# Kernel tuning notes

Measured on AMD Instinct MI355X. Metric: run time of the kernel, lower is better.

Reference implementation:

```python
import jax, jax.numpy as jnp
import numpy as np

B = 131072
SD, AD, HID = 24, 8, 32
NH = SD + AD            # n_heads = 32
UNITS = HID * NH        # 1024


def _xavier(k, shape):
    fan_in, fan_out = shape[-2], shape[-1]
    lim = float(np.sqrt(6.0 / (fan_in + fan_out)))
    return jax.random.uniform(k, shape, jnp.float32, -lim, lim)


def setup_inputs() -> dict:
    key = jax.random.key(0)
    ks = jax.random.split(key, 8)
    return dict(
        state=jax.random.normal(ks[0], (B, SD), jnp.float32),
        action=jax.random.normal(ks[1], (B, AD), jnp.float32),
        # ripple layer 1: per-head Linear(NH -> HID), gate logits init 0 (init_prob=0.5)
        W1=_xavier(ks[2], (NH, NH, HID)), b1=jnp.zeros((NH, HID), jnp.float32), g1=jnp.zeros((NH,), jnp.float32),
        # ripple layer 2: per-head Linear(UNITS -> HID)
        W2=_xavier(ks[3], (NH, UNITS, HID)), b2=jnp.zeros((NH, HID), jnp.float32), g2=jnp.zeros((NH,), jnp.float32),
        # q_network
        Wq1=_xavier(ks[4], (UNITS, 256)), bq1=jnp.zeros((256,), jnp.float32),
        ln1_g=jnp.ones((256,), jnp.float32), ln1_b=jnp.zeros((256,), jnp.float32),
        Wq2=_xavier(ks[5], (256, 128)), bq2=jnp.zeros((128,), jnp.float32),
        ln2_g=jnp.ones((128,), jnp.float32), ln2_b=jnp.zeros((128,), jnp.float32),
        Wq3=_xavier(ks[6], (128, 1)), bq3=jnp.zeros((1,), jnp.float32),
    )


def _ripple(x, W, b, g):
    # x: [B, D]; W: [H, D, K]; per-head linear + tanh, scaled by per-head sigmoid gate
    h = jnp.tanh(jnp.einsum('bd,hdk->bhk', x, W) + b[None])  # [B, H, K]
    h = h * jax.nn.sigmoid(g)[None, :, None]
    return h.reshape(x.shape[0], -1)  # [B, H*K]


def _ln(x, g, b, eps=1e-5):
    mu = jnp.mean(x, -1, keepdims=True)
    var = jnp.mean((x - mu) ** 2, -1, keepdims=True)
    return (x - mu) * jax.lax.rsqrt(var + eps) * g + b


def reference(state, action, W1, b1, g1, W2, b2, g2,
              Wq1, bq1, ln1_g, ln1_b, Wq2, bq2, ln2_g, ln2_b, Wq3, bq3):
    sa = jnp.concatenate([state, action], axis=1)          # [B, SD+AD]
    x = _ripple(sa, W1, b1, g1)                            # [B, UNITS]
    x = _ripple(x, W2, b2, g2)                             # [B, UNITS]
    h = jax.nn.relu(_ln(x @ Wq1 + bq1, ln1_g, ln1_b))      # [B, 256] (dropout = eval identity)
    h = jax.nn.relu(_ln(h @ Wq2 + bq2, ln2_g, ln2_b))      # [B, 128]
    return h @ Wq3 + bq3                                   # [B, 1]
```

## Files before the change

kernel.cpp:

```cpp
#include <hip/hip_runtime.h>
#include <hip/hip_bf16.h>

typedef _Float16 f16x8 __attribute__((ext_vector_type(8)));
typedef _Float16 f16x4 __attribute__((ext_vector_type(4)));
typedef float f32x4 __attribute__((ext_vector_type(4)));

__device__ __forceinline__ float tanh_fast(float x) {
  float e = __expf(2.0f * x);
  return 1.0f - 2.0f * __builtin_amdgcn_rcpf(e + 1.0f);
}
__device__ __forceinline__ float sigmoid_fast(float x) {
  return __builtin_amdgcn_rcpf(1.0f + __expf(-x));
}

__global__ __launch_bounds__(256) void prep_weights(
    const float* __restrict__ W1, const float* __restrict__ W2,
    const float* __restrict__ Wq1, const float* __restrict__ Wq2,
    _Float16* __restrict__ V1p, _Float16* __restrict__ V2p,
    _Float16* __restrict__ T1p, _Float16* __restrict__ T2p) {
  __shared__ float S[32 * 33];
  int b = blockIdx.x, t = threadIdx.x;
  if (b < 2624) {
    const float* in; _Float16* out; int N, nc0, tile;
    if (b < 2048) {
      int h = b >> 6, rem = b & 63, ntl = rem >> 5, kt = rem & 31;
      in = W2 + (size_t)h * 32768 + (size_t)kt * 32 * 32;
      N = 32; nc0 = ntl * 16;
      out = V2p; tile = kt * 64 + (h * 2 + ntl);
    } else if (b < 2560) {
      int i = b - 2048, nt = i >> 5, kt = i & 31;
      in = Wq1 + (size_t)kt * 32 * 256; N = 256; nc0 = nt * 16;
      out = T1p; tile = kt * 16 + nt;
    } else {
      int i = b - 2560, nt = i >> 3, kt = i & 7;
      in = Wq2 + (size_t)kt * 32 * 128; N = 128; nc0 = nt * 16;
      out = T2p; tile = nt * 8 + kt;
    }
    if (t < 128) {
      int r = t >> 2, c4 = (t & 3) * 4;
      const float4 v = *(const float4*)(in + (size_t)r * N + nc0 + c4);
      S[r * 17 + c4 + 0] = v.x; S[r * 17 + c4 + 1] = v.y;
      S[r * 17 + c4 + 2] = v.z; S[r * 17 + c4 + 3] = v.w;
    }
    __syncthreads();
    if (t < 128) {
      int w2 = t >> 6, l = t & 63, q = l >> 4, l15 = l & 15;
      f16x4 o;
#pragma unroll
      for (int jj = 0; jj < 4; ++jj)
        o[jj] = (_Float16)S[(q * 8 + w2 * 4 + jj) * 17 + l15];
      *(f16x4*)(out + (size_t)tile * 512 + l * 8 + w2 * 4) = o;
    }
  } else {
    int h = b - 2624;
    const float* in = W1 + h * 1024;
    int cc = t & 31, rr8 = t >> 5;
#pragma unroll
    for (int p = 0; p < 4; ++p) {
      int r = rr8 + p * 8;
      S[cc * 33 + r] = in[r * 32 + cc];
    }
    __syncthreads();
    if (t < 128) {
      int ntl = t >> 6, l = t & 63, q = l >> 4, l15 = l & 15;
      f16x8 o;
#pragma unroll
      for (int j = 0; j < 8; ++j)
        o[j] = (_Float16)S[(ntl * 16 + l15) * 33 + q * 8 + j];
      *(f16x8*)(V1p + (size_t)(h * 2 + ntl) * 512 + l * 8) = o;
    }
  }
}

__global__ __launch_bounds__(256) void k1_ripple1(
    const float* __restrict__ state, const float* __restrict__ action,
    const _Float16* __restrict__ v1p, const float* __restrict__ b1,
    const float* __restrict__ g1, _Float16* __restrict__ x1p, int gro,
    int NRT, int xcdMatch) {
  __shared__ __align__(16) _Float16 SM[128 * 68];
  int g = blockIdx.x, bn, bm;
  if (xcdMatch) { int x = g & 7, r = g >> 3; bn = r & 7; bm = x + 8 * (r >> 3); }
  else { bn = g & 7; bm = g >> 3; }
  int t = threadIdx.x, w = t >> 6, l = t & 63, q = l >> 4, l15 = l & 15;
  int n0 = bn * 128, m0 = bm * 128;

  {
    int r = t >> 1, half = t & 1;
    size_t grow = (size_t)(gro + m0 + r);
    float v[16];
    if (half == 0) {
      const float4* sp = (const float4*)(state + grow * 24);
      ((float4*)v)[0] = sp[0]; ((float4*)v)[1] = sp[1];
      ((float4*)v)[2] = sp[2]; ((float4*)v)[3] = sp[3];
    } else {
      const float4* sp = (const float4*)(state + grow * 24 + 16);
      ((float4*)v)[0] = sp[0]; ((float4*)v)[1] = sp[1];
      const float4* ap = (const float4*)(action + grow * 8);
      ((float4*)v)[2] = ap[0]; ((float4*)v)[3] = ap[1];
    }
    f16x8 h0, h1;
#pragma unroll
    for (int j = 0; j < 8; ++j) { h0[j] = (_Float16)v[j]; h1[j] = (_Float16)v[8 + j]; }
    *(f16x8*)&SM[r * 40 + half * 16] = h0;
    *(f16x8*)&SM[r * 40 + half * 16 + 8] = h1;
  }
  __syncthreads();

  int wr = w >> 1, wc = w & 1;
  f16x8 af[4], bf[4];
#pragma unroll
  for (int mi = 0; mi < 4; ++mi)
    af[mi] = *(const f16x8*)&SM[(wr * 64 + mi * 16 + l15) * 40 + q * 8];
#pragma unroll
  for (int ni = 0; ni < 4; ++ni)
    bf[ni] = *(const f16x8*)(v1p + (size_t)(bn * 8 + wc * 4 + ni) * 512 + l * 8);

  f32x4 acc[4][4] = {};
#pragma unroll
  for (int mi = 0; mi < 4; ++mi)
#pragma unroll
    for (int ni = 0; ni < 4; ++ni)
      acc[mi][ni] = __builtin_amdgcn_mfma_f32_16x16x32_f16(af[mi], bf[ni], acc[mi][ni], 0, 0, 0);

  for (int p = 0; p < 2; ++p) {
    __syncthreads();
    if (wc == p) {
#pragma unroll
      for (int ni = 0; ni < 4; ++ni) {
        int col = n0 + p * 64 + ni * 16 + l15;
        float sg = sigmoid_fast(g1[col >> 5]);
        float bias = b1[col];
#pragma unroll
        for (int mi = 0; mi < 4; ++mi)
#pragma unroll
          for (int r = 0; r < 4; ++r) {
            int rl = wr * 64 + mi * 16 + q * 4 + r;
            SM[rl * 68 + ni * 16 + l15] = (_Float16)(tanh_fast(acc[mi][ni][r] + bias) * sg);
          }
      }
    }
    __syncthreads();
#pragma unroll
    for (int i = 0; i < 4; ++i) {
      int c = t + i * 256;
      int kcL = c >> 9, rt = (c >> 6) & 7, ll = c & 63;
      int qq = ll >> 4, ll15 = ll & 15;
      int base = (rt * 16 + ll15) * 68 + kcL * 32 + qq * 8;
      union { f16x8 v; f16x4 h[2]; } u;
      u.h[0] = *(const f16x4*)&SM[base];
      u.h[1] = *(const f16x4*)&SM[base + 4];
      int kc = bn * 4 + p * 2 + kcL;
      *(f16x8*)(x1p + ((size_t)kc * NRT + (m0 >> 4) + rt) * 512 + ll * 8) = u.v;
    }
  }
}

__global__ __launch_bounds__(256, 2) void k2_ripple2(
    const _Float16* __restrict__ x1p, const _Float16* __restrict__ v2p,
    const float* __restrict__ b2, const float* __restrict__ g2,
    _Float16* __restrict__ x2p, int nbm, int NRT) {
  __shared__ __align__(16) _Float16 EP[4 * 64 * 36];
  int g = blockIdx.x;
  int bn, bm;
  if ((nbm & 7) == 0) {
    int x = g & 7, j = g >> 3, jj = j >> 2, nJ = nbm >> 3;
    bn = j & 3; bm = x + 8 * (nJ - 1 - jj);
  } else { bn = g & 3; bm = g >> 2; }
  int t = threadIdx.x, w = t >> 6, l = t & 63, q = l >> 4, l15 = l & 15;
  int wr = w >> 1, wc = w & 1;
  int rt0 = bm * 8 + wr * 4;
  int nt0 = bn * 16 + wc * 8;
  f32x4 acc[4][8] = {};

  const size_t aStep = (size_t)NRT * 512;
  const _Float16* aP = x1p + (size_t)rt0 * 512 + (size_t)l * 8;
  const _Float16* bP = v2p + (size_t)nt0 * 512 + (size_t)l * 8;

  f16x8 a0[4], a1[4], b0[8], b1[8];
#pragma unroll
  for (int mi = 0; mi < 4; ++mi) a0[mi] = *(const f16x8*)(aP + mi * 512);
#pragma unroll
  for (int ni = 0; ni < 8; ++ni) b0[ni] = *(const f16x8*)(bP + ni * 512);
#pragma unroll
  for (int mi = 0; mi < 4; ++mi) a1[mi] = *(const f16x8*)(aP + aStep + mi * 512);
#pragma unroll
  for (int ni = 0; ni < 8; ++ni) b1[ni] = *(const f16x8*)(bP + 32768 + ni * 512);
  aP += 2 * aStep; bP += 65536;

  for (int kt = 0; kt < 32; kt += 2) {
#pragma unroll
    for (int mi = 0; mi < 4; ++mi)
#pragma unroll
      for (int ni = 0; ni < 8; ++ni)
        acc[mi][ni] = __builtin_amdgcn_mfma_f32_16x16x32_f16(a0[mi], b0[ni], acc[mi][ni], 0, 0, 0);
    if (kt < 30) {
#pragma unroll
      for (int mi = 0; mi < 4; ++mi) a0[mi] = *(const f16x8*)(aP + mi * 512);
#pragma unroll
      for (int ni = 0; ni < 8; ++ni) b0[ni] = *(const f16x8*)(bP + ni * 512);
    }
#pragma unroll
    for (int mi = 0; mi < 4; ++mi)
#pragma unroll
      for (int ni = 0; ni < 8; ++ni)
        acc[mi][ni] = __builtin_amdgcn_mfma_f32_16x16x32_f16(a1[mi], b1[ni], acc[mi][ni], 0, 0, 0);
    if (kt < 30) {
#pragma unroll
      for (int mi = 0; mi < 4; ++mi) a1[mi] = *(const f16x8*)(aP + aStep + mi * 512);
#pragma unroll
      for (int ni = 0; ni < 8; ++ni) b1[ni] = *(const f16x8*)(bP + 32768 + ni * 512);
      aP += 2 * aStep; bP += 65536;
    }
  }

  _Float16* EPw = EP + w * (64 * 36);
  for (int kcg = 0; kcg < 4; ++kcg) {
#pragma unroll
    for (int np = 0; np < 2; ++np) {
      int ni = kcg * 2 + np;
      int col = (nt0 + ni) * 16 + l15;
      float sg = sigmoid_fast(g2[col >> 5]);
      float bias = b2[col];
#pragma unroll
      for (int mi = 0; mi < 4; ++mi)
#pragma unroll
        for (int r = 0; r < 4; ++r) {
          int row = mi * 16 + q * 4 + r;
          EPw[row * 36 + np * 16 + l15] = (_Float16)(tanh_fast(acc[mi][ni][r] + bias) * sg);
        }
    }
#pragma unroll
    for (int rt = 0; rt < 4; ++rt) {
      int base = (rt * 16 + l15) * 36 + q * 8;
      union { f16x8 v; f16x4 h[2]; } u;
      u.h[0] = *(const f16x4*)&EPw[base];
      u.h[1] = *(const f16x4*)&EPw[base + 4];
      int kc = (nt0 >> 1) + kcg;
      *(f16x8*)(x2p + ((size_t)kc * NRT + rt0 + rt) * 512 + l * 8) = u.v;
    }
  }
}

__global__ __launch_bounds__(512, 3) void k3_head(
    const _Float16* __restrict__ x2p, const _Float16* __restrict__ t1p,
    const _Float16* __restrict__ t2p,
    const float* __restrict__ bq1, const float* __restrict__ ln1g, const float* __restrict__ ln1b,
    const float* __restrict__ bq2, const float* __restrict__ ln2g, const float* __restrict__ ln2b,
    const float* __restrict__ wq3, const float* __restrict__ bq3,
    float* __restrict__ out, int NRT, int SROWS) {
  __shared__ __align__(16) _Float16 y1h[128 * 264];
  __shared__ float redA[128 * 4], redB[128 * 4];
  __shared__ float meanv[128], rstdv[128];
  int bm = blockIdx.x;
  int t = threadIdx.x, w = t >> 6, l = t & 63, q = l >> 4, l15 = l & 15;
  int wr = w >> 2, wc = w & 3;

  int gt = bm * 8;
  int slice = 0;
  if (gt >= NRT) { slice = 1; gt -= NRT; }
  int rt0 = gt + wr * 4;

  f32x4 acc[4][4] = {};
  const size_t aStep = (size_t)NRT * 512;
  const _Float16* aP = x2p + (size_t)slice * SROWS * 1024 + (size_t)rt0 * 512 + (size_t)l * 8;
  const _Float16* bP = t1p + (size_t)(wc * 4) * 512 + (size_t)l * 8;

  f16x8 a0[4], a1[4], b0[4], b1[4];
#pragma unroll
  for (int mi = 0; mi < 4; ++mi) a0[mi] = *(const f16x8*)(aP + mi * 512);
#pragma unroll
  for (int ni = 0; ni < 4; ++ni) b0[ni] = *(const f16x8*)(bP + ni * 512);
#pragma unroll
  for (int mi = 0; mi < 4; ++mi) a1[mi] = *(const f16x8*)(aP + aStep + mi * 512);
#pragma unroll
  for (int ni = 0; ni < 4; ++ni) b1[ni] = *(const f16x8*)(bP + 8192 + ni * 512);
  aP += 2 * aStep; bP += 16384;

  for (int kt = 0; kt < 32; kt += 2) {
#pragma unroll
    for (int mi = 0; mi < 4; ++mi)
#pragma unroll
      for (int ni = 0; ni < 4; ++ni)
        acc[mi][ni] = __builtin_amdgcn_mfma_f32_16x16x32_f16(a0[mi], b0[ni], acc[mi][ni], 0, 0, 0);
    if (kt < 30) {
#pragma unroll
      for (int mi = 0; mi < 4; ++mi) a0[mi] = *(const f16x8*)(aP + mi * 512);
#pragma unroll
      for (int ni = 0; ni < 4; ++ni) b0[ni] = *(const f16x8*)(bP + ni * 512);
    }
#pragma unroll
    for (int mi = 0; mi < 4; ++mi)
#pragma unroll
      for (int ni = 0; ni < 4; ++ni)
        acc[mi][ni] = __builtin_amdgcn_mfma_f32_16x16x32_f16(a1[mi], b1[ni], acc[mi][ni], 0, 0, 0);
    if (kt < 30) {
#pragma unroll
      for (int mi = 0; mi < 4; ++mi) a1[mi] = *(const f16x8*)(aP + aStep + mi * 512);
#pragma unroll
      for (int ni = 0; ni < 4; ++ni) b1[ni] = *(const f16x8*)(bP + 8192 + ni * 512);
      aP += 2 * aStep; bP += 16384;
    }
  }

#pragma unroll
  for (int ni = 0; ni < 4; ++ni) {
    int col = wc * 64 + ni * 16 + l15;
    float b = bq1[col];
#pragma unroll
    for (int mi = 0; mi < 4; ++mi)
#pragma unroll
      for (int r = 0; r < 4; ++r) acc[mi][ni][r] += b;
  }
#pragma unroll
  for (int mi = 0; mi < 4; ++mi)
#pragma unroll
    for (int r = 0; r < 4; ++r) {
      int row = wr * 64 + mi * 16 + q * 4 + r;
      float s = 0.f, sq = 0.f;
#pragma unroll
      for (int ni = 0; ni < 4; ++ni) { float v = acc[mi][ni][r]; s += v; sq += v * v; }
#pragma unroll
      for (int off = 1; off < 16; off <<= 1) { s += __shfl_xor(s, off); sq += __shfl_xor(sq, off); }
      if (l15 == 0) { redA[row * 4 + wc] = s; redB[row * 4 + wc] = sq; }
    }
  __syncthreads();
  if (t < 128) {
    float s  = redA[t * 4] + redA[t * 4 + 1] + redA[t * 4 + 2] + redA[t * 4 + 3];
    float sq = redB[t * 4] + redB[t * 4 + 1] + redB[t * 4 + 2] + redB[t * 4 + 3];
    float mean = s * (1.0f / 256.0f);
    float var = sq * (1.0f / 256.0f) - mean * mean;
    meanv[t] = mean; rstdv[t] = rsqrtf(var + 1e-5f);
  }
  __syncthreads();
#pragma unroll
  for (int mi = 0; mi < 4; ++mi)
#pragma unroll
    for (int ni = 0; ni < 4; ++ni)
#pragma unroll
      for (int r = 0; r < 4; ++r) {
        int row = wr * 64 + mi * 16 + q * 4 + r;
        int col = wc * 64 + ni * 16 + l15;
        float y = (acc[mi][ni][r] - meanv[row]) * rstdv[row] * ln1g[col] + ln1b[col];
        y = fmaxf(y, 0.f);
        y1h[row * 264 + col] = (_Float16)y;
      }
  __syncthreads();

  f32x4 a2[4][2] = {};
  for (int kt = 0; kt < 8; ++kt) {
    f16x8 af2[4];
#pragma unroll
    for (int mi = 0; mi < 4; ++mi)
      af2[mi] = *(const f16x8*)&y1h[(wr * 64 + mi * 16 + l15) * 264 + kt * 32 + q * 8];
#pragma unroll
    for (int ni = 0; ni < 2; ++ni) {
      f16x8 bf = *(const f16x8*)(t2p + (size_t)(wc * 2 + ni) * 4096 + kt * 512 + l * 8);
#pragma unroll
      for (int mi = 0; mi < 4; ++mi)
        a2[mi][ni] = __builtin_amdgcn_mfma_f32_16x16x32_f16(af2[mi], bf, a2[mi][ni], 0, 0, 0);
    }
  }
#pragma unroll
  for (int ni = 0; ni < 2; ++ni) {
    int col = wc * 32 + ni * 16 + l15;
    float b = bq2[col];
#pragma unroll
    for (int mi = 0; mi < 4; ++mi)
#pragma unroll
      for (int r = 0; r < 4; ++r) a2[mi][ni][r] += b;
  }
  __syncthreads();
#pragma unroll
  for (int mi = 0; mi < 4; ++mi)
#pragma unroll
    for (int r = 0; r < 4; ++r) {
      int row = wr * 64 + mi * 16 + q * 4 + r;
      float s = 0.f, sq = 0.f;
#pragma unroll
      for (int ni = 0; ni < 2; ++ni) { float v = a2[mi][ni][r]; s += v; sq += v * v; }
#pragma unroll
      for (int off = 1; off < 16; off <<= 1) { s += __shfl_xor(s, off); sq += __shfl_xor(sq, off); }
      if (l15 == 0) { redA[row * 4 + wc] = s; redB[row * 4 + wc] = sq; }
    }
  __syncthreads();
  if (t < 128) {
    float s  = redA[t * 4] + redA[t * 4 + 1] + redA[t * 4 + 2] + redA[t * 4 + 3];
    float sq = redB[t * 4] + redB[t * 4 + 1] + redB[t * 4 + 2] + redB[t * 4 + 3];
    float mean = s * (1.0f / 128.0f);
    float var = sq * (1.0f / 128.0f) - mean * mean;
    meanv[t] = mean; rstdv[t] = rsqrtf(var + 1e-5f);
  }
  __syncthreads();
#pragma unroll
  for (int mi = 0; mi < 4; ++mi)
#pragma unroll
    for (int r = 0; r < 4; ++r) {
      int row = wr * 64 + mi * 16 + q * 4 + r;
      float pr = 0.f;
#pragma unroll
      for (int ni = 0; ni < 2; ++ni) {
        int col = wc * 32 + ni * 16 + l15;
        float y = (a2[mi][ni][r] - meanv[row]) * rstdv[row] * ln2g[col] + ln2b[col];
        y = fmaxf(y, 0.f);
        pr += y * wq3[col];
      }
#pragma unroll
      for (int off = 1; off < 16; off <<= 1) pr += __shfl_xor(pr, off);
      if (l15 == 0) redA[row * 4 + wc] = pr;
    }
  __syncthreads();
  if (t < 128)
    out[bm * 128 + t] = redA[t * 4] + redA[t * 4 + 1] + redA[t * 4 + 2] + redA[t * 4 + 3] + bq3[0];
}

extern "C" void kernel_launch(void* const* d_in, const int* in_sizes, int n_in,
                              void* d_out, int out_size, void* d_ws, size_t ws_size,
                              hipStream_t stream) {
  const float* state  = (const float*)d_in[0];
  const float* action = (const float*)d_in[1];
  const float* W1  = (const float*)d_in[2];
  const float* b1  = (const float*)d_in[3];
  const float* g1  = (const float*)d_in[4];
  const float* W2  = (const float*)d_in[5];
  const float* b2  = (const float*)d_in[6];
  const float* g2  = (const float*)d_in[7];
  const float* Wq1 = (const float*)d_in[8];
  const float* bq1 = (const float*)d_in[9];
  const float* ln1g = (const float*)d_in[10];
  const float* ln1b = (const float*)d_in[11];
  const float* Wq2 = (const float*)d_in[12];
  const float* bq2 = (const float*)d_in[13];
  const float* ln2g = (const float*)d_in[14];
  const float* ln2b = (const float*)d_in[15];
  const float* Wq3 = (const float*)d_in[16];
  const float* bq3 = (const float*)d_in[17];
  int B = in_sizes[0] / 24;

  char* ws = (char*)d_ws;
  _Float16* V1p = (_Float16*)(ws);
  _Float16* V2p = (_Float16*)(ws + 65536);
  _Float16* T1p = (_Float16*)(ws + 65536 + 2097152);
  _Float16* T2p = (_Float16*)(ws + 65536 + 2097152 + 524288);
  size_t woff = (65536 + 2097152 + 524288 + 65536 + 4095) & ~(size_t)4095;

  size_t avail = ws_size > woff ? ws_size - woff : 0;
  int S, G;
  if (avail >= (size_t)32768 * 2048 * 3) {
    S = 32768; G = 2;
  } else {
    long rows = (long)(avail / 4096);
    if (rows > 32768) rows = 32768;
    rows &= ~127L;
    if (rows < 128) rows = 128;
    S = (int)rows; G = 1;
  }
  _Float16* x1 = (_Float16*)(ws + woff);
  _Float16* x2 = x1 + (size_t)S * 1024;
  int NRT = S / 16;

  prep_weights<<<2656, 256, 0, stream>>>(W1, W2, Wq1, Wq2, V1p, V2p, T1p, T2p);

  int nsl = (B + S - 1) / S;
  for (int i = 0; i < nsl; ++i) {
    int r0 = i * S;
    int Sc = S < (B - r0) ? S : (B - r0);
    int nbm = Sc / 128;
    int xm = (nbm & 7) == 0 ? 1 : 0;
    k1_ripple1<<<dim3(8 * nbm), 256, 0, stream>>>(state, action, V1p, b1, g1, x1, r0,
                                                  NRT, xm);
    k2_ripple2<<<dim3(4 * nbm), 256, 0, stream>>>(x1, V2p, b2, g2,
                                                  x2 + (size_t)(i % G) * S * 1024, nbm, NRT);
    if (i % G == G - 1 || i == nsl - 1) {
      int gstart = (i - i % G) * S;
      int nrows = r0 + Sc - gstart;
      k3_head<<<dim3(nrows / 128), 512, 0, stream>>>(x2, T1p, T2p, bq1, ln1g, ln1b,
                                                     bq2, ln2g, ln2b, Wq3, bq3,
                                                     (float*)d_out + gstart, NRT, S);
    }
  }
}
```

Measured before the change: 636.7 us.

## Fuse ripple layer 1 into ripple layer 2 kernel, keeping x1 in LDS

Merges the two ripple kernels into one 512-thread kernel. Each block recomputes the layer-1 activations for its 128 rows, one 128-column chunk at a time, into double-buffered LDS and feeds them straight into the layer-2 MFMA accumulation. This removes the global write and read of the fp16 x1 intermediate and one kernel launch, and halves the workspace needed per slice. In exchange, layer 1 is recomputed by both column-half blocks, LDS use is much larger and there is a barrier per chunk, which may lower occupancy and latency hiding.

Measured after the change: 608.5 us. 1.05x faster.

```diff
diff --git a/kernel.cpp b/kernel.cpp
--- a/kernel.cpp
+++ b/kernel.cpp
@@ -72,148 +72,123 @@
   }
 }
 
-__global__ __launch_bounds__(256) void k1_ripple1(
+__global__ __launch_bounds__(512, 2) void k12_fused(
     const float* __restrict__ state, const float* __restrict__ action,
     const _Float16* __restrict__ v1p, const float* __restrict__ b1,
-    const float* __restrict__ g1, _Float16* __restrict__ x1p, int gro,
-    int NRT, int xcdMatch) {
-  __shared__ __align__(16) _Float16 SM[128 * 68];
-  int g = blockIdx.x, bn, bm;
-  if (xcdMatch) { int x = g & 7, r = g >> 3; bn = r & 7; bm = x + 8 * (r >> 3); }
-  else { bn = g & 7; bm = g >> 3; }
+    const float* __restrict__ g1,
+    const _Float16* __restrict__ v2p, const float* __restrict__ b2,
+    const float* __restrict__ g2,
+    _Float16* __restrict__ x2p, int gro, int NRT) {
+  __shared__ __align__(16) _Float16 SA[128 * 40];
+  __shared__ __align__(16) _Float16 XF[2 * 16384];
+  __shared__ __align__(16) _Float16 EP[8 * 64 * 36];
+  int g = blockIdx.x;
+  int bn = g & 1, bm = g >> 1;
   int t = threadIdx.x, w = t >> 6, l = t & 63, q = l >> 4, l15 = l & 15;
-  int n0 = bn * 128, m0 = bm * 128;
+  int wrow = w & 1;
+  int cg = w >> 1;
+  int m0 = bm * 128;
 
   {
-    int r = t >> 1, half = t & 1;
+    int r = t >> 2, q4 = t & 3;
     size_t grow = (size_t)(gro + m0 + r);
-    float v[16];
-    if (half == 0) {
-      const float4* sp = (const float4*)(state + grow * 24);
+    float v[8];
+    if (q4 < 3) {
+      const float4* sp = (const float4*)(state + grow * 24 + q4 * 8);
       ((float4*)v)[0] = sp[0]; ((float4*)v)[1] = sp[1];
-      ((float4*)v)[2] = sp[2]; ((float4*)v)[3] = sp[3];
     } else {
-      const float4* sp = (const float4*)(state + grow * 24 + 16);
-      ((float4*)v)[0] = sp[0]; ((float4*)v)[1] = sp[1];
       const float4* ap = (const float4*)(action + grow * 8);
-      ((float4*)v)[2] = ap[0]; ((float4*)v)[3] = ap[1];
-    }
-    f16x8 h0, h1;
-#pragma unroll
-    for (int j = 0; j < 8; ++j) { h0[j] = (_Float16)v[j]; h1[j] = (_Float16)v[8 + j]; }
-    *(f16x8*)&SM[r * 40 + half * 16] = h0;
-    *(f16x8*)&SM[r * 40 + half * 16 + 8] = h1;
-  }
-  __syncthreads();
-
-  int wr = w >> 1, wc = w & 1;
-  f16x8 af[4], bf[4];
-#pragma unroll
-  for (int mi = 0; mi < 4; ++mi)
-    af[mi] = *(const f16x8*)&SM[(wr * 64 + mi * 16 + l15) * 40 + q * 8];
-#pragma unroll
-  for (int ni = 0; ni < 4; ++ni)
-    bf[ni] = *(const f16x8*)(v1p + (size_t)(bn * 8 + wc * 4 + ni) * 512 + l * 8);
-
-  f32x4 acc[4][4] = {};
-#pragma unroll
-  for (int mi = 0; mi < 4; ++mi)
-#pragma unroll
-    for (int ni = 0; ni < 4; ++ni)
-      acc[mi][ni] = __builtin_amdgcn_mfma_f32_16x16x32_f16(af[mi], bf[ni], acc[mi][ni], 0, 0, 0);
-
-  for (int p = 0; p < 2; ++p) {
+      ((float4*)v)[0] = ap[0]; ((float4*)v)[1] = ap[1];
+    }
+    f16x8 h0;
+#pragma unroll
+    for (int j = 0; j < 8; ++j) h0[j] = (_Float16)v[j];
+    *(f16x8*)&SA[r * 40 + q4 * 8] = h0;
+  }
+  __syncthreads();
+
+  f32x4 acc[4][8] = {};
+  _Float16* EPw = EP + w * (64 * 36);
+
+  f16x8 rb[2];
+#pragma unroll
+  for (int ni = 0; ni < 2; ++ni)
+    rb[ni] = *(const f16x8*)(v1p + (size_t)(cg * 2 + ni) * 512 + l * 8);
+
+  const int nt0 = bn * 32 + cg * 8;
+  const _Float16* bBase = v2p + (size_t)nt0 * 512 + (size_t)l * 8;
+
+  for (int kc = 0; kc < 8; ++kc) {
+    f16x8 asa[4];
+#pragma unroll
+    for (int mi = 0; mi < 4; ++mi)
+      asa[mi] = *(const f16x8*)&SA[(wrow * 64 + mi * 16 + l15) * 40 + q * 8];
+    f32x4 a1[4][2] = {};
+#pragma unroll
+    for (int mi = 0; mi < 4; ++mi)
+#pragma unroll
+      for (int ni = 0; ni < 2; ++ni)
+        a1[mi][ni] = __builtin_amdgcn_mfma_f32_16x16x32_f16(asa[mi], rb[ni], a1[mi][ni], 0, 0, 0);
+#pragma unroll
+    for (int ni = 0; ni < 2; ++ni) {
+      int col = kc * 128 + cg * 32 + ni * 16 + l15;
+      float sg = sigmoid_fast(g1[col >> 5]);
+      float bias = b1[col];
+#pragma unroll
+      for (int mi = 0; mi < 4; ++mi)
+#pragma unroll
+        for (int r = 0; r < 4; ++r)
+          EPw[(mi * 16 + q * 4 + r) * 36 + ni * 16 + l15] =
+              (_Float16)(tanh_fast(a1[mi][ni][r] + bias) * sg);
+    }
+    _Float16* buf = XF + (kc & 1) * 16384;
+#pragma unroll
+    for (int rtl = 0; rtl < 4; ++rtl) {
+      int base = (rtl * 16 + l15) * 36 + q * 8;
+      union { f16x8 v; f16x4 h[2]; } u;
+      u.h[0] = *(const f16x4*)&EPw[base];
+      u.h[1] = *(const f16x4*)&EPw[base + 4];
+      *(f16x8*)(buf + ((cg * 8 + wrow * 4 + rtl) * 64 + l) * 8) = u.v;
+    }
     __syncthreads();
-    if (wc == p) {
-#pragma unroll
-      for (int ni = 0; ni < 4; ++ni) {
-        int col = n0 + p * 64 + ni * 16 + l15;
-        float sg = sigmoid_fast(g1[col >> 5]);
-        float bias = b1[col];
-#pragma unroll
-        for (int mi = 0; mi < 4; ++mi)
-#pragma unroll
-          for (int r = 0; r < 4; ++r) {
-            int rl = wr * 64 + mi * 16 + q * 4 + r;
-            SM[rl * 68 + ni * 16 + l15] = (_Float16)(tanh_fast(acc[mi][ni][r] + bias) * sg);
-          }
+
+    if (kc < 7) {
+#pragma unroll
+      for (int ni = 0; ni < 2; ++ni)
+        rb[ni] = *(const f16x8*)(v1p + (size_t)((kc + 1) * 8 + cg * 2 + ni) * 512 + l * 8);
+    }
+    int ktg = kc * 4;
+    f16x8 bb0[8], bb1[8];
+#pragma unroll
+    for (int ni = 0; ni < 8; ++ni)
+      bb0[ni] = *(const f16x8*)(bBase + (size_t)(ktg * 64 + ni) * 512);
+#pragma unroll
+    for (int ni = 0; ni < 8; ++ni)
+      bb1[ni] = *(const f16x8*)(bBase + (size_t)((ktg + 1) * 64 + ni) * 512);
+#pragma unroll
+    for (int ktL = 0; ktL < 4; ++ktL) {
+      f16x8 af[4];
+#pragma unroll
+      for (int mi = 0; mi < 4; ++mi)
+        af[mi] = *(const f16x8*)(buf + ((ktL * 8 + wrow * 4 + mi) * 64 + l) * 8);
+      f16x8* bb = (ktL & 1) ? bb1 : bb0;
+#pragma unroll
+      for (int mi = 0; mi < 4; ++mi)
+#pragma unroll
+        for (int ni = 0; ni < 8; ++ni)
+          acc[mi][ni] = __builtin_amdgcn_mfma_f32_16x16x32_f16(af[mi], bb[ni], acc[mi][ni], 0, 0, 0);
+      if (ktL == 0) {
+#pragma unroll
+        for (int ni = 0; ni < 8; ++ni)
+          bb0[ni] = *(const f16x8*)(bBase + (size_t)((ktg + 2) * 64 + ni) * 512);
+      } else if (ktL == 1) {
+#pragma unroll
+        for (int ni = 0; ni < 8; ++ni)
+          bb1[ni] = *(const f16x8*)(bBase + (size_t)((ktg + 3) * 64 + ni) * 512);
       }
     }
-    __syncthreads();
-#pragma unroll
-    for (int i = 0; i < 4; ++i) {
-      int c = t + i * 256;
-      int kcL = c >> 9, rt = (c >> 6) & 7, ll = c & 63;
-      int qq = ll >> 4, ll15 = ll & 15;
-      int base = (rt * 16 + ll15) * 68 + kcL * 32 + qq * 8;
-      union { f16x8 v; f16x4 h[2]; } u;
-      u.h[0] = *(const f16x4*)&SM[base];
-      u.h[1] = *(const f16x4*)&SM[base + 4];
-      int kc = bn * 4 + p * 2 + kcL;
-      *(f16x8*)(x1p + ((size_t)kc * NRT + (m0 >> 4) + rt) * 512 + ll * 8) = u.v;
-    }
-  }
-}
-
-__global__ __launch_bounds__(256, 2) void k2_ripple2(
-    const _Float16* __restrict__ x1p, const _Float16* __restrict__ v2p,
-    const float* __restrict__ b2, const float* __restrict__ g2,
-    _Float16* __restrict__ x2p, int nbm, int NRT) {
-  __shared__ __align__(16) _Float16 EP[4 * 64 * 36];
-  int g = blockIdx.x;
-  int bn, bm;
-  if ((nbm & 7) == 0) {
-    int x = g & 7, j = g >> 3, jj = j >> 2, nJ = nbm >> 3;
-    bn = j & 3; bm = x + 8 * (nJ - 1 - jj);
-  } else { bn = g & 3; bm = g >> 2; }
-  int t = threadIdx.x, w = t >> 6, l = t & 63, q = l >> 4, l15 = l & 15;
-  int wr = w >> 1, wc = w & 1;
-  int rt0 = bm * 8 + wr * 4;
-  int nt0 = bn * 16 + wc * 8;
-  f32x4 acc[4][8] = {};
-
-  const size_t aStep = (size_t)NRT * 512;
-  const _Float16* aP = x1p + (size_t)rt0 * 512 + (size_t)l * 8;
-  const _Float16* bP = v2p + (size_t)nt0 * 512 + (size_t)l * 8;
-
-  f16x8 a0[4], a1[4], b0[8], b1[8];
-#pragma unroll
-  for (int mi = 0; mi < 4; ++mi) a0[mi] = *(const f16x8*)(aP + mi * 512);
-#pragma unroll
-  for (int ni = 0; ni < 8; ++ni) b0[ni] = *(const f16x8*)(bP + ni * 512);
-#pragma unroll
-  for (int mi = 0; mi < 4; ++mi) a1[mi] = *(const f16x8*)(aP + aStep + mi * 512);
-#pragma unroll
-  for (int ni = 0; ni < 8; ++ni) b1[ni] = *(const f16x8*)(bP + 32768 + ni * 512);
-  aP += 2 * aStep; bP += 65536;
-
-  for (int kt = 0; kt < 32; kt += 2) {
-#pragma unroll
-    for (int mi = 0; mi < 4; ++mi)
-#pragma unroll
-      for (int ni = 0; ni < 8; ++ni)
-        acc[mi][ni] = __builtin_amdgcn_mfma_f32_16x16x32_f16(a0[mi], b0[ni], acc[mi][ni], 0, 0, 0);
-    if (kt < 30) {
-#pragma unroll
-      for (int mi = 0; mi < 4; ++mi) a0[mi] = *(const f16x8*)(aP + mi * 512);
-#pragma unroll
-      for (int ni = 0; ni < 8; ++ni) b0[ni] = *(const f16x8*)(bP + ni * 512);
-    }
-#pragma unroll
-    for (int mi = 0; mi < 4; ++mi)
-#pragma unroll
-      for (int ni = 0; ni < 8; ++ni)
-        acc[mi][ni] = __builtin_amdgcn_mfma_f32_16x16x32_f16(a1[mi], b1[ni], acc[mi][ni], 0, 0, 0);
-    if (kt < 30) {
-#pragma unroll
-      for (int mi = 0; mi < 4; ++mi) a1[mi] = *(const f16x8*)(aP + aStep + mi * 512);
-#pragma unroll
-      for (int ni = 0; ni < 8; ++ni) b1[ni] = *(const f16x8*)(bP + 32768 + ni * 512);
-      aP += 2 * aStep; bP += 65536;
-    }
-  }
-
-  _Float16* EPw = EP + w * (64 * 36);
+  }
+
   for (int kcg = 0; kcg < 4; ++kcg) {
 #pragma unroll
     for (int np = 0; np < 2; ++np) {
@@ -224,19 +199,19 @@
 #pragma unroll
       for (int mi = 0; mi < 4; ++mi)
 #pragma unroll
-        for (int r = 0; r < 4; ++r) {
-          int row = mi * 16 + q * 4 + r;
-          EPw[row * 36 + np * 16 + l15] = (_Float16)(tanh_fast(acc[mi][ni][r] + bias) * sg);
-        }
-    }
-#pragma unroll
-    for (int rt = 0; rt < 4; ++rt) {
-      int base = (rt * 16 + l15) * 36 + q * 8;
+        for (int r = 0; r < 4; ++r)
+          EPw[(mi * 16 + q * 4 + r) * 36 + np * 16 + l15] =
+              (_Float16)(tanh_fast(acc[mi][ni][r] + bias) * sg);
+    }
+#pragma unroll
+    for (int rtl = 0; rtl < 4; ++rtl) {
+      int base = (rtl * 16 + l15) * 36 + q * 8;
       union { f16x8 v; f16x4 h[2]; } u;
       u.h[0] = *(const f16x4*)&EPw[base];
       u.h[1] = *(const f16x4*)&EPw[base + 4];
-      int kc = (nt0 >> 1) + kcg;
-      *(f16x8*)(x2p + ((size_t)kc * NRT + rt0 + rt) * 512 + l * 8) = u.v;
+      int kc2 = (nt0 >> 1) + kcg;
+      int rt = bm * 8 + wrow * 4 + rtl;
+      *(f16x8*)(x2p + ((size_t)kc2 * NRT + rt) * 512 + l * 8) = u.v;
     }
   }
 }
@@ -445,17 +420,16 @@
 
   size_t avail = ws_size > woff ? ws_size - woff : 0;
   int S, G;
-  if (avail >= (size_t)32768 * 2048 * 3) {
+  if (avail >= (size_t)32768 * 2048 * 2) {
     S = 32768; G = 2;
   } else {
-    long rows = (long)(avail / 4096);
+    long rows = (long)(avail / 2048);
     if (rows > 32768) rows = 32768;
     rows &= ~127L;
     if (rows < 128) rows = 128;
     S = (int)rows; G = 1;
   }
-  _Float16* x1 = (_Float16*)(ws + woff);
-  _Float16* x2 = x1 + (size_t)S * 1024;
+  _Float16* x2 = (_Float16*)(ws + woff);
   int NRT = S / 16;
 
   prep_weights<<<2656, 256, 0, stream>>>(W1, W2, Wq1, Wq2, V1p, V2p, T1p, T2p);
@@ -465,11 +439,9 @@
     int r0 = i * S;
     int Sc = S < (B - r0) ? S : (B - r0);
     int nbm = Sc / 128;
-    int xm = (nbm & 7) == 0 ? 1 : 0;
-    k1_ripple1<<<dim3(8 * nbm), 256, 0, stream>>>(state, action, V1p, b1, g1, x1, r0,
-                                                  NRT, xm);
-    k2_ripple2<<<dim3(4 * nbm), 256, 0, stream>>>(x1, V2p, b2, g2,
-                                                  x2 + (size_t)(i % G) * S * 1024, nbm, NRT);
+    k12_fused<<<dim3(2 * nbm), 512, 0, stream>>>(state, action, V1p, b1, g1,
+                                                 V2p, b2, g2,
+                                                 x2 + (size_t)(i % G) * S * 1024, r0, NRT);
     if (i % G == G - 1 || i == nsl - 1) {
       int gstart = (i - i % G) * S;
       int nrows = r0 + Sc - gstart;
```
